# Kernel tuning notes

Measured on AMD Instinct MI355X. Metric: run time of the kernel, lower is better.

The kernel has to match this reference:

```python
import jax, jax.numpy as jnp
import numpy as np

LOC = 200 * 200 + 1   # location vocab
E = 100               # loc_emb_size
H = 100               # hidden_neurons (== input size of STLSTM)
D = 12                # temporal/spatial slot embedding dim
NSLOT = 92


def setup_inputs() -> dict:
    key = jax.random.key(0)
    ks = jax.random.split(key, 24)
    B, T = 1024, 256
    inp = {}
    inp["traj"] = jax.random.randint(ks[0], (B, T), 0, LOC)
    inp["lennew"] = jax.random.randint(ks[1], (B, T), 0, T)
    inp["traj_len"] = 255  # static scalar (loop runs traj_len+1 steps)
    inp["tu"] = jax.random.randint(ks[2], (B, T), 0, NSLOT)
    inp["tl"] = jax.random.randint(ks[3], (B, T), 0, NSLOT)
    inp["tu_slot"] = jax.random.randint(ks[4], (B, T), 0, NSLOT)
    inp["tl_slot"] = jax.random.randint(ks[5], (B, T), 0, NSLOT)
    inp["su"] = jax.random.randint(ks[6], (B, T), 0, NSLOT)
    inp["sl"] = jax.random.randint(ks[7], (B, T), 0, NSLOT)
    inp["su_slot"] = jax.random.randint(ks[8], (B, T), 0, NSLOT)
    inp["sl_slot"] = jax.random.randint(ks[9], (B, T), 0, NSLOT)
    # learned parameters
    inp["emb_loc"] = jax.random.normal(ks[10], (LOC, E), jnp.float32) * 0.02
    inp["emb_t"] = jax.random.normal(ks[11], (NSLOT, D), jnp.float32) * 0.02
    inp["emb_s"] = jax.random.normal(ks[12], (NSLOT, D), jnp.float32) * 0.02
    inp["W_ih"] = jax.random.normal(ks[13], (E, 4 * H), jnp.float32) * 0.05
    inp["W_hh"] = jax.random.normal(ks[14], (H, 4 * H), jnp.float32) * 0.05
    inp["b"] = jnp.zeros((4 * H,), jnp.float32)
    inp["W_xt"] = jax.random.normal(ks[15], (E, H), jnp.float32) * 0.05
    inp["W_tt"] = jax.random.normal(ks[16], (D, H), jnp.float32) * 0.05
    inp["b_t"] = jnp.zeros((H,), jnp.float32)
    inp["W_xs"] = jax.random.normal(ks[17], (E, H), jnp.float32) * 0.05
    inp["W_ss"] = jax.random.normal(ks[18], (D, H), jnp.float32) * 0.05
    inp["b_s"] = jnp.zeros((H,), jnp.float32)
    return inp


def reference(traj, lennew, traj_len, tu, tl, tu_slot, tl_slot, su, sl,
              su_slot, sl_slot, emb_loc, emb_t, emb_s, W_ih, W_hh, b,
              W_xt, W_tt, b_t, W_xs, W_ss, b_s):
    steps = int(traj_len) + 1  # static python int -> static slice
    x = emb_loc[traj[:, :steps]]            # [B, S, E] (dropout is identity in eval)
    dtype = x.dtype

    def interp(up_e, low_e, up_d, low_d):
        # linear interpolation between upper/lower slot embeddings
        up = up_d[:, :steps].astype(dtype)[..., None]
        low = low_d[:, :steps].astype(dtype)[..., None]
        return (up * low_e + low * up_e) / jnp.maximum(up + low, 1.0)

    Tq = interp(emb_t[tu[:, :steps]], emb_t[tl[:, :steps]], tu_slot, tl_slot)  # [B,S,D]
    Sq = interp(emb_s[su[:, :steps]], emb_s[sl[:, :steps]], su_slot, sl_slot)  # [B,S,D]

    B = traj.shape[0]
    h0 = jnp.zeros((B, H), dtype)
    c0 = jnp.zeros((B, H), dtype)
    xs = (x.swapaxes(0, 1), Tq.swapaxes(0, 1), Sq.swapaxes(0, 1))  # time-major

    def step(carry, inp):
        h, c = carry
        xt, tg, sg = inp
        gates = xt @ W_ih + h @ W_hh + b           # [B, 4H]
        i, f, g, o = jnp.split(gates, 4, axis=-1)
        i = jax.nn.sigmoid(i)
        f = jax.nn.sigmoid(f)
        g = jnp.tanh(g)
        o = jax.nn.sigmoid(o)
        tgate = jax.nn.sigmoid(xt @ W_xt + tg @ W_tt + b_t)  # temporal gate
        sgate = jax.nn.sigmoid(xt @ W_xs + sg @ W_ss + b_s)  # spatial gate
        c = f * c + i * tgate * sgate * g
        h = o * jnp.tanh(c)
        return (h, c), None

    (h, c), _ = jax.lax.scan(step, (h0, c0), xs)
    # model returns h at index traj_len, which is the final hidden state
    return h
```

## Files before the change

kernel.cpp:

```cpp
#include <hip/hip_runtime.h>

#define B_    1024
#define T_    256
#define LOCN  40001
#define E_    100
#define H_    100
#define NC    600

constexpr int PROWS = 16;
constexpr int PPAD  = 20;

__global__ __launch_bounds__(320) void proj_loc_kernel(
    const float* __restrict__ emb_loc,
    const float* __restrict__ W_ih,
    const float* __restrict__ W_xt,
    const float* __restrict__ W_xs,
    const float* __restrict__ b,
    const float* __restrict__ b_t,
    const float* __restrict__ b_s,
    float* __restrict__ P)
{
    __shared__ __attribute__((aligned(16))) float aT[E_][PPAD];
    const int tid  = threadIdx.x;
    const int row0 = blockIdx.x * PROWS;

    for (int i = tid; i < PROWS * E_; i += 320) {
        int r = i / E_, k = i - r * E_;
        int rr = row0 + r;
        float v = 0.f;
        if (rr < LOCN) v = emb_loc[rr * E_ + k];
        aT[k][r] = v;
    }
    __syncthreads();
    if (tid >= 300) return;

    for (int cc = 0; cc < 2; ++cc) {
        const int c = tid + cc * 300;
        const float* wp; int stride; float bias;
        if (c < 400)      { wp = W_ih + c;         stride = 400; bias = b[c]; }
        else if (c < 500) { wp = W_xt + (c - 400); stride = 100; bias = b_t[c - 400]; }
        else              { wp = W_xs + (c - 500); stride = 100; bias = b_s[c - 500]; }

        float acc[PROWS];
        #pragma unroll
        for (int r = 0; r < PROWS; ++r) acc[r] = bias;

        for (int k = 0; k < E_; ++k) {
            float w = wp[(size_t)k * stride];
            #pragma unroll
            for (int r = 0; r < PROWS; ++r) acc[r] += aT[k][r] * w;
        }
        #pragma unroll
        for (int r = 0; r < PROWS; ++r) {
            int rr = row0 + r;
            if (rr < LOCN) P[(size_t)rr * NC + c] = acc[r];
        }
    }
}

__global__ void proj_ts_kernel(
    const float* __restrict__ emb_t, const float* __restrict__ emb_s,
    const float* __restrict__ W_tt,  const float* __restrict__ W_ss,
    float* __restrict__ P_t, float* __restrict__ P_s)
{
    int idx = blockIdx.x * 256 + threadIdx.x;
    if (idx >= 2 * 92 * H_) return;
    int which = idx / (92 * H_);
    int rem   = idx - which * (92 * H_);
    int r = rem / H_, c = rem - r * H_;
    const float* e = which ? emb_s : emb_t;
    const float* W = which ? W_ss : W_tt;
    float acc = 0.f;
    #pragma unroll
    for (int k = 0; k < 12; ++k) acc += e[r * 12 + k] * W[k * H_ + c];
    (which ? P_s : P_t)[rem] = acc;
}

constexpr int RB = 4;
constexpr int NT = 704;

__global__ __launch_bounds__(NT, 3) void lstm_rec_kernel(
    const int* __restrict__ traj,
    const int* __restrict__ traj_len_p,
    const int* __restrict__ tu,      const int* __restrict__ tl,
    const int* __restrict__ tu_slot, const int* __restrict__ tl_slot,
    const int* __restrict__ su,      const int* __restrict__ sl,
    const int* __restrict__ su_slot, const int* __restrict__ sl_slot,
    const float* __restrict__ P,
    const float* __restrict__ P_t,
    const float* __restrict__ P_s,
    const float* __restrict__ W_hh,
    float* __restrict__ out)
{
    __shared__ __attribute__((aligned(16))) float h_lds[RB][H_];
    __shared__ float gates_lds[RB][400];
    __shared__ float tg_lds[RB][H_];
    __shared__ float sg_lds[RB][H_];
    __shared__ int   loc_lds[2][RB];

    const int tid = threadIdx.x;
    const int b0  = blockIdx.x * RB;
    int steps = traj_len_p[0] + 1;
    if (steps > T_) steps = T_;

    float w[H_];
    if (tid < 400) {
        #pragma unroll
        for (int k = 0; k < H_; ++k) w[k] = W_hh[k * 400 + tid];
        ((float*)h_lds)[tid] = 0.f;
    }
    if (tid < RB) loc_lds[0][tid] = traj[(b0 + tid) * T_];

    const int er = tid / 100;
    const int eh = tid - er * 100;
    float c_reg = 0.f, hval = 0.f;
    __syncthreads();

    for (int t = 0; t < steps; ++t) {
        const int buf = t & 1;

        if (tid >= 700) {
            int r = tid - 700;
            if (t + 1 < steps) loc_lds[buf ^ 1][r] = traj[(b0 + r) * T_ + t + 1];
        }

        if (tid < 400) {
            const int n = tid;
            float gacc[RB];
            #pragma unroll
            for (int r = 0; r < RB; ++r)
                gacc[r] = P[(size_t)loc_lds[buf][r] * NC + n];

            float acc[RB] = {0.f, 0.f, 0.f, 0.f};
            #pragma unroll
            for (int k4 = 0; k4 < H_ / 4; ++k4) {
                #pragma unroll
                for (int r = 0; r < RB; ++r) {
                    float4 hv = *(const float4*)(&h_lds[r][k4 * 4]);
                    acc[r] += hv.x * w[k4 * 4 + 0];
                    acc[r] += hv.y * w[k4 * 4 + 1];
                    acc[r] += hv.z * w[k4 * 4 + 2];
                    acc[r] += hv.w * w[k4 * 4 + 3];
                }
            }
            const bool isg = (n >= 200 && n < 300);
            #pragma unroll
            for (int r = 0; r < RB; ++r) {
                float v  = acc[r] + gacc[r];
                float xx = isg ? 2.f * v : v;
                float s  = 1.f / (1.f + expf(-xx));
                gates_lds[r][n] = isg ? (2.f * s - 1.f) : s;
            }
        }

        if (tid >= 448 && tid < 648) {
            const int  ch   = tid - 448;
            const bool is_t = ch < 100;
            const int  hx   = is_t ? ch : ch - 100;
            const int* up_a = is_t ? tu_slot : su_slot;
            const int* lo_a = is_t ? tl_slot : sl_slot;
            const int* ui_a = is_t ? tu : su;
            const int* li_a = is_t ? tl : sl;
            const float* Pq = is_t ? P_t : P_s;
            float* dst      = is_t ? &tg_lds[0][0] : &sg_lds[0][0];
            #pragma unroll
            for (int r = 0; r < RB; ++r) {
                const int off = (b0 + r) * T_ + t;
                float gp  = P[(size_t)loc_lds[buf][r] * NC + 400 + ch];
                float up  = (float)up_a[off];
                float low = (float)lo_a[off];
                int   ui  = ui_a[off], li = li_a[off];
                float iv  = (up * Pq[li * H_ + hx] + low * Pq[ui * H_ + hx])
                            / fmaxf(up + low, 1.f);
                float pre = gp + iv;
                dst[r * H_ + hx] = 1.f / (1.f + expf(-pre));
            }
        }
        __syncthreads();

        if (tid < 400) {
            float i_g = gates_lds[er][eh];
            float f_g = gates_lds[er][100 + eh];
            float g_g = gates_lds[er][200 + eh];
            float o_g = gates_lds[er][300 + eh];
            float tsg = tg_lds[er][eh] * sg_lds[er][eh];
            c_reg = f_g * c_reg + i_g * tsg * g_g;
            hval  = o_g * tanhf(c_reg);
            h_lds[er][eh] = hval;
        }
        __syncthreads();
    }

    if (tid < 400) out[b0 * H_ + tid] = hval;
}

extern "C" void kernel_launch(void* const* d_in, const int* in_sizes, int n_in,
                              void* d_out, int out_size, void* d_ws, size_t ws_size,
                              hipStream_t stream) {
    const int*   traj     = (const int*)  d_in[0];
    const int*   traj_len = (const int*)  d_in[2];
    const int*   tu       = (const int*)  d_in[3];
    const int*   tl       = (const int*)  d_in[4];
    const int*   tu_slot  = (const int*)  d_in[5];
    const int*   tl_slot  = (const int*)  d_in[6];
    const int*   su       = (const int*)  d_in[7];
    const int*   sl       = (const int*)  d_in[8];
    const int*   su_slot  = (const int*)  d_in[9];
    const int*   sl_slot  = (const int*)  d_in[10];
    const float* emb_loc  = (const float*)d_in[11];
    const float* emb_t    = (const float*)d_in[12];
    const float* emb_s    = (const float*)d_in[13];
    const float* W_ih     = (const float*)d_in[14];
    const float* W_hh     = (const float*)d_in[15];
    const float* b        = (const float*)d_in[16];
    const float* W_xt     = (const float*)d_in[17];
    const float* W_tt     = (const float*)d_in[18];
    const float* b_t      = (const float*)d_in[19];
    const float* W_xs     = (const float*)d_in[20];
    const float* W_ss     = (const float*)d_in[21];
    const float* b_s      = (const float*)d_in[22];

    float* P   = (float*)d_ws;
    float* P_t = P + (size_t)LOCN * NC;
    float* P_s = P_t + 92 * H_;

    proj_loc_kernel<<<(LOCN + PROWS - 1) / PROWS, 320, 0, stream>>>(
        emb_loc, W_ih, W_xt, W_xs, b, b_t, b_s, P);
    proj_ts_kernel<<<(2 * 92 * H_ + 255) / 256, 256, 0, stream>>>(
        emb_t, emb_s, W_tt, W_ss, P_t, P_s);
    lstm_rec_kernel<<<B_ / RB, NT, 0, stream>>>(
        traj, traj_len, tu, tl, tu_slot, tl_slot, su, sl, su_slot, sl_slot,
        P, P_t, P_s, W_hh, (float*)d_out);
}
```

Before: 831.5 us.

## Restructure LSTM recurrence with double-buffered state, shuffled gates and prefetched inputs

The recurrent kernel now handles 2 batch rows per block instead of 4, with 448 threads. It interleaves the four gate columns so that each hidden unit's i/f/g/o values sit in adjacent lanes and are combined with wave shuffles. This removes the gates LDS buffer and one of the two barriers per step. The h, temporal and spatial buffers are double-buffered, and trajectory indices, projected rows and slot data are prefetched one to two steps ahead in registers so global latency is off the critical path. The projection kernel also doubles its rows per block, at the cost of more registers and a more complex, macro-unrolled schedule.

```diff
diff --git a/kernel.cpp b/kernel.cpp
--- a/kernel.cpp
+++ b/kernel.cpp
@@ -7,8 +7,8 @@
 #define H_    100
 #define NC    600
 
-constexpr int PROWS = 16;
-constexpr int PPAD  = 20;
+constexpr int PROWS = 32;
+constexpr int PPAD  = 36;
 
 __global__ __launch_bounds__(320) void proj_loc_kernel(
     const float* __restrict__ emb_loc,
@@ -46,9 +46,9 @@
         for (int r = 0; r < PROWS; ++r) acc[r] = bias;
 
         for (int k = 0; k < E_; ++k) {
-            float w = wp[(size_t)k * stride];
+            float wv = wp[(size_t)k * stride];
             #pragma unroll
-            for (int r = 0; r < PROWS; ++r) acc[r] += aT[k][r] * w;
+            for (int r = 0; r < PROWS; ++r) acc[r] += aT[k][r] * wv;
         }
         #pragma unroll
         for (int r = 0; r < PROWS; ++r) {
@@ -76,10 +76,10 @@
     (which ? P_s : P_t)[rem] = acc;
 }
 
-constexpr int RB = 4;
-constexpr int NT = 704;
-
-__global__ __launch_bounds__(NT, 3) void lstm_rec_kernel(
+constexpr int RB = 2;
+constexpr int NT = 448;
+
+__global__ __launch_bounds__(NT, 4) void lstm_rec_kernel(
     const int* __restrict__ traj,
     const int* __restrict__ traj_len_p,
     const int* __restrict__ tu,      const int* __restrict__ tl,
@@ -92,106 +92,158 @@
     const float* __restrict__ W_hh,
     float* __restrict__ out)
 {
-    __shared__ __attribute__((aligned(16))) float h_lds[RB][H_];
-    __shared__ float gates_lds[RB][400];
-    __shared__ float tg_lds[RB][H_];
-    __shared__ float sg_lds[RB][H_];
-    __shared__ int   loc_lds[2][RB];
+    __shared__ __attribute__((aligned(16))) float h_lds[2][RB][H_];
+    __shared__ float tg_lds[2][RB][H_];
+    __shared__ float sg_lds[2][RB][H_];
 
     const int tid = threadIdx.x;
     const int b0  = blockIdx.x * RB;
+    const int tb0 = b0 * T_;
+    const int tb1 = tb0 + T_;
     int steps = traj_len_p[0] + 1;
     if (steps > T_) steps = T_;
+    steps = __builtin_amdgcn_readfirstlane(steps);
+
+    const int gi = tid & 3;
+    const int q  = tid >> 2;
+    const int n  = gi * 100 + q;
+
+    const int  tsr  = tid / 200;
+    const int  ch   = tid - tsr * 200;
+    const bool is_t = ch < 100;
+    const int  hx   = is_t ? ch : ch - 100;
+    const int* up_a = is_t ? tu_slot : su_slot;
+    const int* lo_a = is_t ? tl_slot : sl_slot;
+    const int* ui_a = is_t ? tu : su;
+    const int* li_a = is_t ? tl : sl;
+    const float* Pq = is_t ? P_t : P_s;
+    const int  tso  = (tsr == 1) ? tb1 : tb0;
+    const int  gcol = 400 + ch;
+    float* tsw = (is_t ? &tg_lds[0][0][0] : &sg_lds[0][0][0]) + tsr * H_ + hx;
 
     float w[H_];
     if (tid < 400) {
         #pragma unroll
-        for (int k = 0; k < H_; ++k) w[k] = W_hh[k * 400 + tid];
-        ((float*)h_lds)[tid] = 0.f;
-    }
-    if (tid < RB) loc_lds[0][tid] = traj[(b0 + tid) * T_];
-
-    const int er = tid / 100;
-    const int eh = tid - er * 100;
-    float c_reg = 0.f, hval = 0.f;
+        for (int k = 0; k < H_; ++k) w[k] = W_hh[k * 400 + n];
+    }
+    if (tid < RB * H_) ((float*)h_lds)[tid] = 0.f;
+
+    float c0 = 0.f, c1 = 0.f;
+    int lB0 = 0, lB1 = 0, lC0 = 0, lC1 = 0;
+    int uA = 0, lsA = 0, uiA = 0, liA = 0; float gpA = 0.f;
+    int uB = 0, lsB = 0, uiB = 0, liB = 0; float gpB = 0.f;
+    float gA0 = 0.f, gA1 = 0.f, gB0 = 0.f, gB1 = 0.f;
+
+    if (tid < 400) {
+        const int t1 = (steps > 1) ? 1 : 0;
+        const int t2 = (steps > 2) ? 2 : steps - 1;
+        const int lA0 = __builtin_amdgcn_readfirstlane(traj[tb0]);
+        const int lA1 = __builtin_amdgcn_readfirstlane(traj[tb1]);
+        lB0 = __builtin_amdgcn_readfirstlane(traj[tb0 + t1]);
+        lB1 = __builtin_amdgcn_readfirstlane(traj[tb1 + t1]);
+        lC0 = __builtin_amdgcn_readfirstlane(traj[tb0 + t2]);
+        lC1 = __builtin_amdgcn_readfirstlane(traj[tb1 + t2]);
+        gA0 = P[(size_t)lA0 * NC + n];
+        gA1 = P[(size_t)lA1 * NC + n];
+        {
+            const int off0 = tso;
+            const float fu = (float)up_a[off0], fl = (float)lo_a[off0];
+            const int   iu = ui_a[off0],       il = li_a[off0];
+            const float gp = P[(size_t)((tsr == 1) ? lA1 : lA0) * NC + gcol];
+            const float iv = (fu * Pq[il * H_ + hx] + fl * Pq[iu * H_ + hx])
+                             / fmaxf(fu + fl, 1.f);
+            tsw[0] = 1.f / (1.f + expf(-(gp + iv)));
+        }
+        {
+            const int off1 = tso + t1;
+            uA = up_a[off1]; lsA = lo_a[off1]; uiA = ui_a[off1]; liA = li_a[off1];
+            gpA = P[(size_t)((tsr == 1) ? lB1 : lB0) * NC + gcol];
+        }
+    }
     __syncthreads();
 
-    for (int t = 0; t < steps; ++t) {
-        const int buf = t & 1;
-
-        if (tid >= 700) {
-            int r = tid - 700;
-            if (t + 1 < steps) loc_lds[buf ^ 1][r] = traj[(b0 + r) * T_ + t + 1];
-        }
-
-        if (tid < 400) {
-            const int n = tid;
-            float gacc[RB];
-            #pragma unroll
-            for (int r = 0; r < RB; ++r)
-                gacc[r] = P[(size_t)loc_lds[buf][r] * NC + n];
-
-            float acc[RB] = {0.f, 0.f, 0.f, 0.f};
-            #pragma unroll
-            for (int k4 = 0; k4 < H_ / 4; ++k4) {
-                #pragma unroll
-                for (int r = 0; r < RB; ++r) {
-                    float4 hv = *(const float4*)(&h_lds[r][k4 * 4]);
-                    acc[r] += hv.x * w[k4 * 4 + 0];
-                    acc[r] += hv.y * w[k4 * 4 + 1];
-                    acc[r] += hv.z * w[k4 * 4 + 2];
-                    acc[r] += hv.w * w[k4 * 4 + 3];
-                }
-            }
-            const bool isg = (n >= 200 && n < 300);
-            #pragma unroll
-            for (int r = 0; r < RB; ++r) {
-                float v  = acc[r] + gacc[r];
-                float xx = isg ? 2.f * v : v;
-                float s  = 1.f / (1.f + expf(-xx));
-                gates_lds[r][n] = isg ? (2.f * s - 1.f) : s;
-            }
-        }
-
-        if (tid >= 448 && tid < 648) {
-            const int  ch   = tid - 448;
-            const bool is_t = ch < 100;
-            const int  hx   = is_t ? ch : ch - 100;
-            const int* up_a = is_t ? tu_slot : su_slot;
-            const int* lo_a = is_t ? tl_slot : sl_slot;
-            const int* ui_a = is_t ? tu : su;
-            const int* li_a = is_t ? tl : sl;
-            const float* Pq = is_t ? P_t : P_s;
-            float* dst      = is_t ? &tg_lds[0][0] : &sg_lds[0][0];
-            #pragma unroll
-            for (int r = 0; r < RB; ++r) {
-                const int off = (b0 + r) * T_ + t;
-                float gp  = P[(size_t)loc_lds[buf][r] * NC + 400 + ch];
-                float up  = (float)up_a[off];
-                float low = (float)lo_a[off];
-                int   ui  = ui_a[off], li = li_a[off];
-                float iv  = (up * Pq[li * H_ + hx] + low * Pq[ui * H_ + hx])
-                            / fmaxf(up + low, 1.f);
-                float pre = gp + iv;
-                dst[r * H_ + hx] = 1.f / (1.f + expf(-pre));
-            }
-        }
-        __syncthreads();
-
-        if (tid < 400) {
-            float i_g = gates_lds[er][eh];
-            float f_g = gates_lds[er][100 + eh];
-            float g_g = gates_lds[er][200 + eh];
-            float o_g = gates_lds[er][300 + eh];
-            float tsg = tg_lds[er][eh] * sg_lds[er][eh];
-            c_reg = f_g * c_reg + i_g * tsg * g_g;
-            hval  = o_g * tanhf(c_reg);
-            h_lds[er][eh] = hval;
-        }
-        __syncthreads();
-    }
-
-    if (tid < 400) out[b0 * H_ + tid] = hval;
+#define LSTM_STEP(tt, CUR, uC,lsC,uiC,liC,gpC,  uN,lsN,uiN,liN,gpN,  gC0,gC1, gN0,gN1)  \
+  {                                                                                     \
+    constexpr int CB = (CUR);                                                           \
+    constexpr int NB = CB ^ 1;                                                          \
+    if (tid < 400) {                                                                    \
+      const int tD = ((tt) + 3 < steps) ? (tt) + 3 : steps - 1;                         \
+      const int t2 = ((tt) + 2 < steps) ? (tt) + 2 : steps - 1;                         \
+      const int nD0 = __builtin_amdgcn_readfirstlane(traj[tb0 + tD]);                   \
+      const int nD1 = __builtin_amdgcn_readfirstlane(traj[tb1 + tD]);                   \
+                                \
+      gN0 = P[(size_t)lB0 * NC + n];                                                    \
+      gN1 = P[(size_t)lB1 * NC + n];                                                    \
+                             \
+      const int off2 = tso + t2;                                                        \
+      uN  = up_a[off2]; lsN = lo_a[off2]; uiN = ui_a[off2]; liN = li_a[off2];           \
+      gpN = P[(size_t)((tsr == 1) ? lC1 : lC0) * NC + gcol];                            \
+                    \
+      const float pql = Pq[(liC) * H_ + hx];                                            \
+      const float pqu = Pq[(uiC) * H_ + hx];                                            \
+                                                                          \
+      float acc0 = 0.f, acc1 = 0.f;                                                     \
+      _Pragma("unroll")                                                                 \
+      for (int k4 = 0; k4 < H_ / 4; ++k4) {                                             \
+        const float4 h0 = *(const float4*)(&h_lds[CB][0][k4 * 4]);                      \
+        const float4 h1 = *(const float4*)(&h_lds[CB][1][k4 * 4]);                      \
+        acc0 += h0.x * w[k4*4+0]; acc0 += h0.y * w[k4*4+1];                             \
+        acc0 += h0.z * w[k4*4+2]; acc0 += h0.w * w[k4*4+3];                             \
+        acc1 += h1.x * w[k4*4+0]; acc1 += h1.y * w[k4*4+1];                             \
+        acc1 += h1.z * w[k4*4+2]; acc1 += h1.w * w[k4*4+3];                             \
+      }                                                                                 \
+                                                                       \
+      const bool isg = (gi == 2);                                                       \
+      const float v0 = acc0 + gC0;                                                      \
+      const float v1 = acc1 + gC1;                                                      \
+      const float x0 = isg ? 2.f * v0 : v0;                                             \
+      const float x1 = isg ? 2.f * v1 : v1;                                             \
+      const float s0 = 1.f / (1.f + expf(-x0));                                         \
+      const float s1 = 1.f / (1.f + expf(-x1));                                         \
+      const float a0 = isg ? 2.f * s0 - 1.f : s0;                                       \
+      const float a1 = isg ? 2.f * s1 - 1.f : s1;                                       \
+                                        \
+      const float f0 = __shfl_xor(a0, 1);                                               \
+      const float g0 = __shfl_xor(a0, 2);                                               \
+      const float o0 = __shfl_xor(f0, 2);                                               \
+      const float f1 = __shfl_xor(a1, 1);                                               \
+      const float g1 = __shfl_xor(a1, 2);                                               \
+      const float o1 = __shfl_xor(f1, 2);                                               \
+      if (gi == 0) {                                \
+        const float ts0 = tg_lds[CB][0][q] * sg_lds[CB][0][q];                          \
+        const float ts1 = tg_lds[CB][1][q] * sg_lds[CB][1][q];                          \
+        c0 = f0 * c0 + a0 * ts0 * g0;                                                   \
+        c1 = f1 * c1 + a1 * ts1 * g1;                                                   \
+        h_lds[NB][0][q] = o0 * tanhf(c0);                                               \
+        h_lds[NB][1][q] = o1 * tanhf(c1);                                               \
+      }                                                                                 \
+                                          \
+      {                                                                                 \
+        const float fu = (float)(uC), fl = (float)(lsC);                                \
+        const float iv = (fu * pql + fl * pqu) / fmaxf(fu + fl, 1.f);                   \
+        tsw[NB * (RB * H_)] = 1.f / (1.f + expf(-((gpC) + iv)));                        \
+      }                                                                                 \
+      lB0 = lC0; lB1 = lC1; lC0 = nD0; lC1 = nD1;                                       \
+    }                                                                                   \
+               \
+    asm volatile("s_waitcnt lgkmcnt(0)\n\ts_barrier" ::: "memory");                     \
+  }
+
+    int t = 0;
+    for (; t + 1 < steps; t += 2) {
+        LSTM_STEP(t,     0, uA,lsA,uiA,liA,gpA, uB,lsB,uiB,liB,gpB, gA0,gA1, gB0,gB1)
+        LSTM_STEP(t + 1, 1, uB,lsB,uiB,liB,gpB, uA,lsA,uiA,liA,gpA, gB0,gB1, gA0,gA1)
+    }
+    if (t < steps) {
+        LSTM_STEP(t, 0, uA,lsA,uiA,liA,gpA, uB,lsB,uiB,liB,gpB, gA0,gA1, gB0,gB1)
+    }
+#undef LSTM_STEP
+
+    if (tid < RB * H_) {
+        const int r  = tid / H_;
+        const int qq = tid - r * H_;
+        out[(b0 + r) * H_ + qq] = h_lds[steps & 1][r][qq];
+    }
 }
 
 extern "C" void kernel_launch(void* const* d_in, const int* in_sizes, int n_in,
```

New measurement: 1.934 ms. 133% more time.
